# Optimization experiments

Measured on AMD Instinct MI355X. Metric: run time of the kernel, lower is better.

The kernel has to match this reference:

```python
import jax, jax.numpy as jnp
import numpy as np

N_NODES = 100000
N_EDGES = 3200000
F_IN = 128
F_OUT = 128


def setup_inputs() -> dict:
    key = jax.random.key(0)
    k_x, k_r, k_c, k_v, k_w = jax.random.split(key, 5)
    x = jax.random.normal(k_x, (N_NODES, F_IN), dtype=jnp.float32)
    adj_rows = jnp.sort(jax.random.randint(k_r, (N_EDGES,), 0, N_NODES, dtype=jnp.int32))
    adj_cols = jax.random.randint(k_c, (N_EDGES,), 0, N_NODES, dtype=jnp.int32)
    adj_vals = jax.random.uniform(k_v, (N_EDGES,), dtype=jnp.float32)
    # glorot init for W, zeros for bias (as in the original module)
    limit = np.sqrt(6.0 / (F_IN + F_OUT)).astype(np.float32)
    W = jax.random.uniform(k_w, (F_IN, F_OUT), dtype=jnp.float32, minval=-limit, maxval=limit)
    b = jnp.zeros((F_OUT,), dtype=jnp.float32)
    return {"x": x, "adj_rows": adj_rows, "adj_cols": adj_cols,
            "adj_vals": adj_vals, "W": W, "b": b}


def reference(x, adj_rows, adj_cols, adj_vals, W, b):
    # dropout = 0.0 (disabled), sparse_inputs = False, featureless = False
    # pre_sup = x @ W  -- dense feature transform [N, F_out]
    pre_sup = jnp.matmul(x, W)
    # support @ pre_sup -- sparse adjacency SpMM via gather + segment_sum
    msgs = adj_vals[:, None] * pre_sup[adj_cols]        # [E, F_out]
    agg = jax.ops.segment_sum(msgs, adj_rows,
                              num_segments=N_NODES,
                              indices_are_sorted=True)   # [N, F_out]
    out = agg + b
    return jax.nn.relu(out)
```

## Files before the change

kernel.cpp:

```cpp
#include <hip/hip_runtime.h>
#include <cstdint>
#include <cstddef>

#define N_NODES 100000
#define N_EDGES 3200000
#define F_IN 128
#define F_OUT 128
#define KPAD 136

#define ROWPTR_BYTES ((N_NODES + 1) * 4)
#define O_XB   (((ROWPTR_BYTES) + 255) & ~255)
#define XB_BYTES (N_NODES * F_IN * 2)
#define O_AXB  (O_XB + XB_BYTES)
#define AXB_BYTES (N_NODES * F_OUT * 2)
#define O_WT_A (O_AXB + AXB_BYTES)
#define WT_SWZ_BYTES (F_OUT * F_IN * 2)
#define NEED_A ((size_t)(O_WT_A + WT_SWZ_BYTES))
#define O_WT_A2 O_AXB
#define WT_KPAD_BYTES (F_OUT * KPAD * 2)
#define NEED_A2 ((size_t)(O_WT_A2 + WT_KPAD_BYTES))
#define O_WT_B O_XB
#define NEED_B ((size_t)(O_WT_B + WT_KPAD_BYTES))

typedef __attribute__((ext_vector_type(8))) short short8;
typedef __attribute__((ext_vector_type(4))) float f32x4;

__device__ __forceinline__ unsigned short f2bf(float f) {
    union { float f; unsigned u; } v; v.f = f;
    return (unsigned short)((v.u + 0x7FFFu + ((v.u >> 16) & 1u)) >> 16);
}
__device__ __forceinline__ float bflo(unsigned u) {
    union { unsigned u; float f; } v; v.u = u << 16; return v.f;
}
__device__ __forceinline__ float bfhi(unsigned u) {
    union { unsigned u; float f; } v; v.u = u & 0xFFFF0000u; return v.f;
}

__device__ __forceinline__ int lower_bound_i32(const int* __restrict__ a, int n, int key) {
    int lo = 0, hi = n;
    while (lo < hi) {
        int mid = (lo + hi) >> 1;
        if (a[mid] < key) lo = mid + 1; else hi = mid;
    }
    return lo;
}

__global__ __launch_bounds__(256) void build_rowptr_kernel(
    const int* __restrict__ rows, int* __restrict__ rowptr)
{
    const int n = blockIdx.x * 256 + threadIdx.x;
    if (n <= N_NODES) rowptr[n] = lower_bound_i32(rows, N_EDGES, n);
}

__global__ __launch_bounds__(256) void convert_x_kernel(
    const float4* __restrict__ x4, unsigned short* __restrict__ xb)
{
    const unsigned i = blockIdx.x * 256 + threadIdx.x;
    if (i < (N_NODES * F_IN / 8)) {
        const float4 a = x4[2 * i], b = x4[2 * i + 1];
        uint4 p;
        p.x = (unsigned)f2bf(a.x) | ((unsigned)f2bf(a.y) << 16);
        p.y = (unsigned)f2bf(a.z) | ((unsigned)f2bf(a.w) << 16);
        p.z = (unsigned)f2bf(b.x) | ((unsigned)f2bf(b.y) << 16);
        p.w = (unsigned)f2bf(b.z) | ((unsigned)f2bf(b.w) << 16);
        *reinterpret_cast<uint4*>(xb + (size_t)i * 8) = p;
    }
}

__global__ __launch_bounds__(256) void build_wt_swz_kernel(
    const float* __restrict__ W, char* __restrict__ Wt)
{
    const int idx = blockIdx.x * 256 + threadIdx.x;
    if (idx < F_IN * F_OUT) {
        const int c = idx >> 7, k = idx & 127;
        *reinterpret_cast<unsigned short*>(
            Wt + c * 256 + ((k * 2) ^ ((c & 7) << 4))) = f2bf(W[k * F_OUT + c]);
    }
}

__global__ __launch_bounds__(256) void build_wt_kpad_kernel(
    const float* __restrict__ W, unsigned short* __restrict__ Wt)
{
    const int idx = blockIdx.x * 256 + threadIdx.x;
    if (idx < F_IN * F_OUT) {
        const int c = idx >> 7, k = idx & 127;
        Wt[c * KPAD + k] = f2bf(W[k * F_OUT + c]);
    }
}

template<int OUT_MODE>
__global__ __launch_bounds__(256) void spmm_xb_kernel(
    const unsigned* __restrict__ xb,
    const int*      __restrict__ cols,
    const float*    __restrict__ vals,
    const int*      __restrict__ rowptr,
    void*           __restrict__ outp)
{
    const int row  = blockIdx.x * 4 + (threadIdx.x >> 6);
    const int lane = threadIdx.x & 63;
    if (row >= N_NODES) return;

    const int e0 = rowptr[row], e1 = rowptr[row + 1];
    float ax = 0.f, ay = 0.f;

    int e = e0;
    for (; e + 8 <= e1; e += 8) {
        int c[8]; float v[8]; unsigned u[8];
        #pragma unroll
        for (int j = 0; j < 8; ++j) { c[j] = cols[e + j]; v[j] = vals[e + j]; }
        #pragma unroll
        for (int j = 0; j < 8; ++j) u[j] = xb[(unsigned)c[j] * 64u + lane];
        #pragma unroll
        for (int j = 0; j < 8; ++j) {
            ax = fmaf(v[j], bflo(u[j]), ax);
            ay = fmaf(v[j], bfhi(u[j]), ay);
        }
    }
    for (; e < e1; ++e) {
        const float v = vals[e];
        const unsigned u = xb[(unsigned)cols[e] * 64u + lane];
        ax = fmaf(v, bflo(u), ax);
        ay = fmaf(v, bfhi(u), ay);
    }

    if (OUT_MODE == 0) {
        float2 o; o.x = ax; o.y = ay;
        reinterpret_cast<float2*>(outp)[(size_t)row * 64 + lane] = o;
    } else {
        const unsigned p = (unsigned)f2bf(ax) | ((unsigned)f2bf(ay) << 16);
        *reinterpret_cast<unsigned*>(
            (char*)outp + (size_t)row * 256 + ((lane * 4) ^ ((row & 7) << 4))) = p;
    }
}

__global__ __launch_bounds__(256) void gemm_ws_mfma(
    const char*  __restrict__ AXb,
    const char*  __restrict__ Wt,
    const float* __restrict__ bias,
    float*       __restrict__ out)
{
    __shared__ uint4 A_lds4[64 * 16];
    __shared__ uint4 W_lds4[128 * 16];
    const int t  = threadIdx.x;
    const int r0 = blockIdx.x * 64;

    {
        const uint4* As = reinterpret_cast<const uint4*>(AXb + (size_t)blockIdx.x * 16384);
        #pragma unroll
        for (int i = 0; i < 4; ++i) A_lds4[t + 256 * i] = As[t + 256 * i];
        const uint4* Ws = reinterpret_cast<const uint4*>(Wt);
        #pragma unroll
        for (int i = 0; i < 8; ++i) W_lds4[t + 256 * i] = Ws[t + 256 * i];
    }
    __syncthreads();

    const char* A_lds = reinterpret_cast<const char*>(A_lds4);
    const char* W_lds = reinterpret_cast<const char*>(W_lds4);

    const int lane = t & 63;
    const int w    = t >> 6;
    const int lr   = lane & 15;
    const int lg   = lane >> 4;
    const int sw   = (lr & 7) << 4;

    f32x4 acc[8];
    #pragma unroll
    for (int n = 0; n < 8; ++n) acc[n] = (f32x4){0.f, 0.f, 0.f, 0.f};

    const char* Abase = A_lds + (w * 16 + lr) * 256;
    #pragma unroll
    for (int ks = 0; ks < 4; ++ks) {
        const int koff = (ks * 64 + lg * 16) ^ sw;
        const short8 a = *reinterpret_cast<const short8*>(Abase + koff);
        #pragma unroll
        for (int n = 0; n < 8; ++n) {
            const short8 b = *reinterpret_cast<const short8*>(
                W_lds + (n * 16 + lr) * 256 + koff);
            acc[n] = __builtin_amdgcn_mfma_f32_16x16x32_bf16(a, b, acc[n], 0, 0, 0);
        }
    }

    const int row_base = r0 + w * 16 + lg * 4;
    #pragma unroll
    for (int n = 0; n < 8; ++n) {
        const int col = n * 16 + lr;
        const float bb = bias[col];
        #pragma unroll
        for (int reg = 0; reg < 4; ++reg) {
            const int r = row_base + reg;
            if (r < N_NODES)
                out[(size_t)r * F_OUT + col] = fmaxf(acc[n][reg] + bb, 0.f);
        }
    }
}

template<bool USE_ROWPTR>
__global__ __launch_bounds__(256) void spmm_ax_kernel(
    const float* __restrict__ x,
    const int*   __restrict__ rows,
    const int*   __restrict__ cols,
    const float* __restrict__ vals,
    const int*   __restrict__ rowptr,
    float*       __restrict__ out)
{
    const int row  = blockIdx.x * 4 + (threadIdx.x >> 6);
    const int lane = threadIdx.x & 63;
    if (row >= N_NODES) return;

    int e0, e1;
    if (USE_ROWPTR) { e0 = rowptr[row]; e1 = rowptr[row + 1]; }
    else {
        e0 = lower_bound_i32(rows, N_EDGES, row);
        e1 = lower_bound_i32(rows, N_EDGES, row + 1);
    }
    const float2* __restrict__ x2 = reinterpret_cast<const float2*>(x);
    float ax = 0.f, ay = 0.f;
    int e = e0;
    for (; e + 8 <= e1; e += 8) {
        int c[8]; float v[8]; float2 a[8];
        #pragma unroll
        for (int j = 0; j < 8; ++j) { c[j] = cols[e + j]; v[j] = vals[e + j]; }
        #pragma unroll
        for (int j = 0; j < 8; ++j) a[j] = x2[(unsigned)c[j] * 64u + lane];
        #pragma unroll
        for (int j = 0; j < 8; ++j) {
            ax = fmaf(v[j], a[j].x, ax); ay = fmaf(v[j], a[j].y, ay);
        }
    }
    for (; e < e1; ++e) {
        const float v = vals[e];
        const float2 a = x2[(unsigned)cols[e] * 64u + lane];
        ax = fmaf(v, a.x, ax); ay = fmaf(v, a.y, ay);
    }
    float2 o; o.x = ax; o.y = ay;
    reinterpret_cast<float2*>(out)[(size_t)row * 64 + lane] = o;
}

template<bool WT_WS>
__global__ __launch_bounds__(256) void gemm_mfma_bias_relu_inplace(
    float*                __restrict__ out,
    const unsigned short* __restrict__ Wt_ws,
    const float*          __restrict__ W,
    const float*          __restrict__ bias)
{
    __shared__ short A_lds[64][KPAD];
    __shared__ short Wt_lds[F_OUT][KPAD];
    const int t  = threadIdx.x;
    const int r0 = blockIdx.x * 64;
    const int rows_here = (N_NODES - r0 < 64) ? (N_NODES - r0) : 64;
    {
        const float4* __restrict__ A4 =
            reinterpret_cast<const float4*>(out + (size_t)r0 * F_IN);
        const int nA = rows_here * 32;
        for (int i = t; i < nA; i += 256) {
            const int r = i >> 5, q = i & 31;
            const float4 va = A4[i];
            uint2 p;
            p.x = (unsigned)f2bf(va.x) | ((unsigned)f2bf(va.y) << 16);
            p.y = (unsigned)f2bf(va.z) | ((unsigned)f2bf(va.w) << 16);
            *reinterpret_cast<uint2*>(&A_lds[r][q * 4]) = p;
        }
    }
    if (WT_WS) {
        const float4* __restrict__ src = reinterpret_cast<const float4*>(Wt_ws);
        float4* dst = reinterpret_cast<float4*>(&Wt_lds[0][0]);
        for (int i = t; i < (WT_KPAD_BYTES / 16); i += 256) dst[i] = src[i];
    } else {
        if (t < F_OUT)
            for (int k = 0; k < F_IN; ++k)
                Wt_lds[t][k] = (short)f2bf(W[k * F_OUT + t]);
    }
    __syncthreads();

    const int lane = t & 63, w = t >> 6, lr = lane & 15, lg = lane >> 4;
    f32x4 acc[8];
    #pragma unroll
    for (int n = 0; n < 8; ++n) acc[n] = (f32x4){0.f, 0.f, 0.f, 0.f};
    #pragma unroll
    for (int ks = 0; ks < 4; ++ks) {
        const short8 a = *reinterpret_cast<const short8*>(
            &A_lds[w * 16 + lr][ks * 32 + lg * 8]);
        #pragma unroll
        for (int n = 0; n < 8; ++n) {
            const short8 b = *reinterpret_cast<const short8*>(
                &Wt_lds[n * 16 + lr][ks * 32 + lg * 8]);
            acc[n] = __builtin_amdgcn_mfma_f32_16x16x32_bf16(a, b, acc[n], 0, 0, 0);
        }
    }
    const int row_base = r0 + w * 16 + lg * 4;
    #pragma unroll
    for (int n = 0; n < 8; ++n) {
        const int col = n * 16 + lr;
        const float bb = bias[col];
        #pragma unroll
        for (int reg = 0; reg < 4; ++reg) {
            const int r = row_base + reg;
            if (r < N_NODES)
                out[(size_t)r * F_OUT + col] = fmaxf(acc[n][reg] + bb, 0.f);
        }
    }
}

extern "C" void kernel_launch(void* const* d_in, const int* in_sizes, int n_in,
                              void* d_out, int out_size, void* d_ws, size_t ws_size,
                              hipStream_t stream) {
    const float* x    = (const float*)d_in[0];
    const int*   rows = (const int*)  d_in[1];
    const int*   cols = (const int*)  d_in[2];
    const float* vals = (const float*)d_in[3];
    const float* W    = (const float*)d_in[4];
    const float* b    = (const float*)d_in[5];
    float* out = (float*)d_out;
    char*  ws  = (char*)d_ws;

    if (ws_size >= NEED_A) {
        int* rowptr = (int*)ws;
        unsigned short* xb = (unsigned short*)(ws + O_XB);
        char* AXb = ws + O_AXB;
        char* Wt  = ws + O_WT_A;
        build_rowptr_kernel<<<(N_NODES + 256) / 256, 256, 0, stream>>>(rows, rowptr);
        convert_x_kernel<<<(N_NODES * F_IN / 8 + 255) / 256, 256, 0, stream>>>(
            (const float4*)x, xb);
        build_wt_swz_kernel<<<(F_IN * F_OUT + 255) / 256, 256, 0, stream>>>(W, Wt);
        spmm_xb_kernel<1><<<(N_NODES + 3) / 4, 256, 0, stream>>>(
            (const unsigned*)xb, cols, vals, rowptr, AXb);
        gemm_ws_mfma<<<(N_NODES + 63) / 64, 256, 0, stream>>>(AXb, Wt, b, out);
    } else if (ws_size >= NEED_A2) {
        int* rowptr = (int*)ws;
        unsigned short* xb = (unsigned short*)(ws + O_XB);
        unsigned short* Wt = (unsigned short*)(ws + O_WT_A2);
        build_rowptr_kernel<<<(N_NODES + 256) / 256, 256, 0, stream>>>(rows, rowptr);
        convert_x_kernel<<<(N_NODES * F_IN / 8 + 255) / 256, 256, 0, stream>>>(
            (const float4*)x, xb);
        build_wt_kpad_kernel<<<(F_IN * F_OUT + 255) / 256, 256, 0, stream>>>(W, Wt);
        spmm_xb_kernel<0><<<(N_NODES + 3) / 4, 256, 0, stream>>>(
            (const unsigned*)xb, cols, vals, rowptr, out);
        gemm_mfma_bias_relu_inplace<true><<<(N_NODES + 63) / 64, 256, 0, stream>>>(
            out, Wt, nullptr, b);
    } else if (ws_size >= NEED_B) {
        int* rowptr = (int*)ws;
        unsigned short* Wt = (unsigned short*)(ws + O_WT_B);
        build_rowptr_kernel<<<(N_NODES + 256) / 256, 256, 0, stream>>>(rows, rowptr);
        build_wt_kpad_kernel<<<(F_IN * F_OUT + 255) / 256, 256, 0, stream>>>(W, Wt);
        spmm_ax_kernel<true><<<(N_NODES + 3) / 4, 256, 0, stream>>>(
            x, rows, cols, vals, rowptr, out);
        gemm_mfma_bias_relu_inplace<true><<<(N_NODES + 63) / 64, 256, 0, stream>>>(
            out, Wt, nullptr, b);
    } else {
        spmm_ax_kernel<false><<<(N_NODES + 3) / 4, 256, 0, stream>>>(
            x, rows, cols, vals, nullptr, out);
        gemm_mfma_bias_relu_inplace<false><<<(N_NODES + 63) / 64, 256, 0, stream>>>(
            out, nullptr, W, b);
    }
}
```

Measured before the change: 274.8 us.

## Replace LDS-staged swizzled GEMM with direct global MFMA loads and deeper SpMM unroll

The final GEMM no longer stages the aggregated bf16 tile and the transposed weights in LDS with an XOR swizzle. Each wave now loads its MFMA operands straight from global memory, so the SpMM output and weight layouts become linear. The SpMM gather loop unrolls to 16 edges with a 4-edge middle tail to put more loads in flight, and the x conversion now handles 4 floats per thread instead of 8. This drops the LDS copy and the barrier, but W is now re-read from global memory or cache by every wave, and register pressure in the SpMM loop goes up.

```diff
diff --git a/kernel.cpp b/kernel.cpp
--- a/kernel.cpp
+++ b/kernel.cpp
@@ -14,8 +14,8 @@
 #define O_AXB  (O_XB + XB_BYTES)
 #define AXB_BYTES (N_NODES * F_OUT * 2)
 #define O_WT_A (O_AXB + AXB_BYTES)
-#define WT_SWZ_BYTES (F_OUT * F_IN * 2)
-#define NEED_A ((size_t)(O_WT_A + WT_SWZ_BYTES))
+#define WT_LIN_BYTES (F_OUT * F_IN * 2)
+#define NEED_A ((size_t)(O_WT_A + WT_LIN_BYTES))
 #define O_WT_A2 O_AXB
 #define WT_KPAD_BYTES (F_OUT * KPAD * 2)
 #define NEED_A2 ((size_t)(O_WT_A2 + WT_KPAD_BYTES))
@@ -53,28 +53,25 @@
 }
 
 __global__ __launch_bounds__(256) void convert_x_kernel(
-    const float4* __restrict__ x4, unsigned short* __restrict__ xb)
+    const float4* __restrict__ x4, uint2* __restrict__ xb2)
 {
     const unsigned i = blockIdx.x * 256 + threadIdx.x;
-    if (i < (N_NODES * F_IN / 8)) {
-        const float4 a = x4[2 * i], b = x4[2 * i + 1];
-        uint4 p;
+    if (i < (N_NODES * F_IN / 4)) {
+        const float4 a = x4[i];
+        uint2 p;
         p.x = (unsigned)f2bf(a.x) | ((unsigned)f2bf(a.y) << 16);
         p.y = (unsigned)f2bf(a.z) | ((unsigned)f2bf(a.w) << 16);
-        p.z = (unsigned)f2bf(b.x) | ((unsigned)f2bf(b.y) << 16);
-        p.w = (unsigned)f2bf(b.z) | ((unsigned)f2bf(b.w) << 16);
-        *reinterpret_cast<uint4*>(xb + (size_t)i * 8) = p;
-    }
-}
-
-__global__ __launch_bounds__(256) void build_wt_swz_kernel(
-    const float* __restrict__ W, char* __restrict__ Wt)
+        xb2[i] = p;
+    }
+}
+
+__global__ __launch_bounds__(256) void build_wt_lin_kernel(
+    const float* __restrict__ W, unsigned short* __restrict__ Wt)
 {
     const int idx = blockIdx.x * 256 + threadIdx.x;
     if (idx < F_IN * F_OUT) {
         const int c = idx >> 7, k = idx & 127;
-        *reinterpret_cast<unsigned short*>(
-            Wt + c * 256 + ((k * 2) ^ ((c & 7) << 4))) = f2bf(W[k * F_OUT + c]);
+        Wt[idx] = f2bf(W[k * F_OUT + c]);
     }
 }
 
@@ -104,14 +101,26 @@
     float ax = 0.f, ay = 0.f;
 
     int e = e0;
-    for (; e + 8 <= e1; e += 8) {
-        int c[8]; float v[8]; unsigned u[8];
-        #pragma unroll
-        for (int j = 0; j < 8; ++j) { c[j] = cols[e + j]; v[j] = vals[e + j]; }
-        #pragma unroll
-        for (int j = 0; j < 8; ++j) u[j] = xb[(unsigned)c[j] * 64u + lane];
-        #pragma unroll
-        for (int j = 0; j < 8; ++j) {
+    for (; e + 16 <= e1; e += 16) {
+        int c[16]; float v[16]; unsigned u[16];
+        #pragma unroll
+        for (int j = 0; j < 16; ++j) { c[j] = cols[e + j]; v[j] = vals[e + j]; }
+        #pragma unroll
+        for (int j = 0; j < 16; ++j) u[j] = xb[(unsigned)c[j] * 64u + lane];
+        #pragma unroll
+        for (int j = 0; j < 16; ++j) {
+            ax = fmaf(v[j], bflo(u[j]), ax);
+            ay = fmaf(v[j], bfhi(u[j]), ay);
+        }
+    }
+    for (; e + 4 <= e1; e += 4) {
+        int c[4]; float v[4]; unsigned u[4];
+        #pragma unroll
+        for (int j = 0; j < 4; ++j) { c[j] = cols[e + j]; v[j] = vals[e + j]; }
+        #pragma unroll
+        for (int j = 0; j < 4; ++j) u[j] = xb[(unsigned)c[j] * 64u + lane];
+        #pragma unroll
+        for (int j = 0; j < 4; ++j) {
             ax = fmaf(v[j], bflo(u[j]), ax);
             ay = fmaf(v[j], bfhi(u[j]), ay);
         }
@@ -128,59 +137,44 @@
         reinterpret_cast<float2*>(outp)[(size_t)row * 64 + lane] = o;
     } else {
         const unsigned p = (unsigned)f2bf(ax) | ((unsigned)f2bf(ay) << 16);
-        *reinterpret_cast<unsigned*>(
-            (char*)outp + (size_t)row * 256 + ((lane * 4) ^ ((row & 7) << 4))) = p;
-    }
-}
-
-__global__ __launch_bounds__(256) void gemm_ws_mfma(
-    const char*  __restrict__ AXb,
-    const char*  __restrict__ Wt,
-    const float* __restrict__ bias,
-    float*       __restrict__ out)
-{
-    __shared__ uint4 A_lds4[64 * 16];
-    __shared__ uint4 W_lds4[128 * 16];
-    const int t  = threadIdx.x;
-    const int r0 = blockIdx.x * 64;
-
-    {
-        const uint4* As = reinterpret_cast<const uint4*>(AXb + (size_t)blockIdx.x * 16384);
-        #pragma unroll
-        for (int i = 0; i < 4; ++i) A_lds4[t + 256 * i] = As[t + 256 * i];
-        const uint4* Ws = reinterpret_cast<const uint4*>(Wt);
-        #pragma unroll
-        for (int i = 0; i < 8; ++i) W_lds4[t + 256 * i] = Ws[t + 256 * i];
-    }
-    __syncthreads();
-
-    const char* A_lds = reinterpret_cast<const char*>(A_lds4);
-    const char* W_lds = reinterpret_cast<const char*>(W_lds4);
-
+        reinterpret_cast<unsigned*>(outp)[(size_t)row * 64 + lane] = p;
+    }
+}
+
+__global__ __launch_bounds__(256) void gemm_direct_mfma(
+    const unsigned short* __restrict__ AXb,
+    const unsigned short* __restrict__ Wt,
+    const float*          __restrict__ bias,
+    float*                __restrict__ out)
+{
+    const int t    = threadIdx.x;
     const int lane = t & 63;
     const int w    = t >> 6;
     const int lr   = lane & 15;
     const int lg   = lane >> 4;
-    const int sw   = (lr & 7) << 4;
+    const int row0 = blockIdx.x * 64 + w * 16;
+
+    const short* __restrict__ Arow =
+        reinterpret_cast<const short*>(AXb) + (size_t)(row0 + lr) * F_IN + lg * 8;
+    const short* __restrict__ Wbase =
+        reinterpret_cast<const short*>(Wt) + lr * F_IN + lg * 8;
 
     f32x4 acc[8];
     #pragma unroll
     for (int n = 0; n < 8; ++n) acc[n] = (f32x4){0.f, 0.f, 0.f, 0.f};
 
-    const char* Abase = A_lds + (w * 16 + lr) * 256;
     #pragma unroll
     for (int ks = 0; ks < 4; ++ks) {
-        const int koff = (ks * 64 + lg * 16) ^ sw;
-        const short8 a = *reinterpret_cast<const short8*>(Abase + koff);
+        const short8 a = *reinterpret_cast<const short8*>(Arow + ks * 32);
         #pragma unroll
         for (int n = 0; n < 8; ++n) {
             const short8 b = *reinterpret_cast<const short8*>(
-                W_lds + (n * 16 + lr) * 256 + koff);
+                Wbase + n * 16 * F_IN + ks * 32);
             acc[n] = __builtin_amdgcn_mfma_f32_16x16x32_bf16(a, b, acc[n], 0, 0, 0);
         }
     }
 
-    const int row_base = r0 + w * 16 + lg * 4;
+    const int row_base = row0 + lg * 4;
     #pragma unroll
     for (int n = 0; n < 8; ++n) {
         const int col = n * 16 + lr;
@@ -206,7 +200,6 @@
     const int row  = blockIdx.x * 4 + (threadIdx.x >> 6);
     const int lane = threadIdx.x & 63;
     if (row >= N_NODES) return;
-
     int e0, e1;
     if (USE_ROWPTR) { e0 = rowptr[row]; e1 = rowptr[row + 1]; }
     else {
@@ -315,23 +308,23 @@
 
     if (ws_size >= NEED_A) {
         int* rowptr = (int*)ws;
-        unsigned short* xb = (unsigned short*)(ws + O_XB);
-        char* AXb = ws + O_AXB;
-        char* Wt  = ws + O_WT_A;
+        unsigned short* xb  = (unsigned short*)(ws + O_XB);
+        unsigned short* AXb = (unsigned short*)(ws + O_AXB);
+        unsigned short* Wt  = (unsigned short*)(ws + O_WT_A);
         build_rowptr_kernel<<<(N_NODES + 256) / 256, 256, 0, stream>>>(rows, rowptr);
-        convert_x_kernel<<<(N_NODES * F_IN / 8 + 255) / 256, 256, 0, stream>>>(
-            (const float4*)x, xb);
-        build_wt_swz_kernel<<<(F_IN * F_OUT + 255) / 256, 256, 0, stream>>>(W, Wt);
+        convert_x_kernel<<<(N_NODES * F_IN / 4 + 255) / 256, 256, 0, stream>>>(
+            (const float4*)x, (uint2*)xb);
+        build_wt_lin_kernel<<<(F_IN * F_OUT + 255) / 256, 256, 0, stream>>>(W, Wt);
         spmm_xb_kernel<1><<<(N_NODES + 3) / 4, 256, 0, stream>>>(
             (const unsigned*)xb, cols, vals, rowptr, AXb);
-        gemm_ws_mfma<<<(N_NODES + 63) / 64, 256, 0, stream>>>(AXb, Wt, b, out);
+        gemm_direct_mfma<<<(N_NODES + 63) / 64, 256, 0, stream>>>(AXb, Wt, b, out);
     } else if (ws_size >= NEED_A2) {
         int* rowptr = (int*)ws;
         unsigned short* xb = (unsigned short*)(ws + O_XB);
         unsigned short* Wt = (unsigned short*)(ws + O_WT_A2);
         build_rowptr_kernel<<<(N_NODES + 256) / 256, 256, 0, stream>>>(rows, rowptr);
-        convert_x_kernel<<<(N_NODES * F_IN / 8 + 255) / 256, 256, 0, stream>>>(
-            (const float4*)x, xb);
+        convert_x_kernel<<<(N_NODES * F_IN / 4 + 255) / 256, 256, 0, stream>>>(
+            (const float4*)x, (uint2*)xb);
         build_wt_kpad_kernel<<<(F_IN * F_OUT + 255) / 256, 256, 0, stream>>>(W, Wt);
         spmm_xb_kernel<0><<<(N_NODES + 3) / 4, 256, 0, stream>>>(
             (const unsigned*)xb, cols, vals, rowptr, out);
```

After: 283.8 us. +3.3%, slower.
